# Kernel tuning notes

Hardware: AMD Instinct MI355X
Metric: run time of the kernel (lower is better)

Reference implementation:

```python
import jax, jax.numpy as jnp
import numpy as np

NUM_HEADS = 12
KEEP_RATE = 0.7
EPS = 1e-5  # torch nn.LayerNorm default


def layernorm(x, w, b):
    m = x.mean(-1, keepdims=True)
    v = ((x - m) ** 2).mean(-1, keepdims=True)
    return (x - m) * jax.lax.rsqrt(v + EPS) * w + b


def complement_idx(idx, dim):
    # idx: (B, L) top-k indices into [0, dim). Returns (B, dim-L) sorted complement,
    # matching EViT's scatter-zeros-then-sort trick.
    a = jnp.broadcast_to(jnp.arange(dim, dtype=idx.dtype), idx.shape[:-1] + (dim,))
    masked = jax.vmap(lambda ar, ix: ar.at[ix].set(0))(a, idx)
    n_idx = idx.shape[-1]
    return jnp.sort(masked, axis=-1)[..., n_idx:]


def setup_inputs() -> dict:
    key = jax.random.key(0)
    ks = jax.random.split(key, 8)
    B, N, C = 128, 197, 768
    H = 4 * C
    std = 0.02
    return {
        "x": jax.random.normal(ks[0], (B, N, C), jnp.float32),
        "norm1_w": jnp.ones((C,), jnp.float32),
        "norm1_b": jnp.zeros((C,), jnp.float32),
        "qkv_w": jax.random.normal(ks[1], (C, 3 * C), jnp.float32) * std,  # qkv_bias=False
        "proj_w": jax.random.normal(ks[2], (C, C), jnp.float32) * std,
        "proj_b": jnp.zeros((C,), jnp.float32),
        "norm2_w": jnp.ones((C,), jnp.float32),
        "norm2_b": jnp.zeros((C,), jnp.float32),
        "fc1_w": jax.random.normal(ks[3], (C, H), jnp.float32) * std,
        "fc1_b": jnp.zeros((H,), jnp.float32),
        "fc2_w": jax.random.normal(ks[4], (H, C), jnp.float32) * std,
        "fc2_b": jnp.zeros((C,), jnp.float32),
    }


def reference(x, norm1_w, norm1_b, qkv_w, proj_w, proj_b,
              norm2_w, norm2_b, fc1_w, fc1_b, fc2_w, fc2_b):
    B, N, C = x.shape
    h = NUM_HEADS
    d = C // h
    scale = d ** -0.5

    # ---- Attention (eval mode, no dropout) ----
    xn = layernorm(x, norm1_w, norm1_b)
    qkv = (xn @ qkv_w).reshape(B, N, 3, h, d).transpose(2, 0, 3, 1, 4)
    q, k, v = qkv[0], qkv[1], qkv[2]  # (B, h, N, d)
    attn = jax.nn.softmax(jnp.einsum('bhqd,bhkd->bhqk', q, k) * scale, axis=-1)
    out = jnp.einsum('bhqk,bhkd->bhqd', attn, v).transpose(0, 2, 1, 3).reshape(B, N, C)
    x = x + (out @ proj_w + proj_b)

    # ---- Top-k token selection (keep_rate < 1) ----
    left = int(np.ceil(KEEP_RATE * (N - 1)))          # 138 kept patch tokens
    cls_attn = attn[:, :, 0, 1:].mean(axis=1)         # (B, N-1)
    _, idx = jax.lax.top_k(cls_attn, left)            # sorted descending, like torch.topk
    compl = complement_idx(idx, N - 1)                # (B, M), M = N-1-left

    non_cls = x[:, 1:]                                # (B, N-1, C)
    gather = lambda arr, ix: jnp.take_along_axis(arr, ix[..., None], axis=1)

    x_others = gather(non_cls, idx)                   # (B, L, C)
    non_topk = gather(non_cls, compl)                 # (B, M, C)
    xo_n = x_others / jnp.linalg.norm(x_others, axis=-1, keepdims=True)
    nt_n = non_topk / jnp.linalg.norm(non_topk, axis=-1, keepdims=True)
    distance = jnp.einsum('bmc,blc->bml', nt_n, xo_n)  # cosine similarity (B, M, L)

    # attention-weighted merge of pruned tokens into nearest kept token
    non_cls_w = non_cls * cls_attn[..., None]
    x_others = gather(non_cls_w, idx)
    non_topk = gather(non_cls_w, compl)
    topk_attn = jnp.take_along_axis(cls_attn, idx, axis=1)       # (B, L)
    non_topk_attn = jnp.take_along_axis(cls_attn, compl, axis=1)  # (B, M)
    node_idx = jnp.argmax(distance, axis=-1)                      # (B, M)

    topk_attn = jax.vmap(lambda t, ni, nt: t.at[ni].add(nt))(topk_attn, node_idx, non_topk_attn)
    x_others = jax.vmap(lambda xo, ni, nt: xo.at[ni].add(nt))(x_others, node_idx, non_topk)
    x_others = x_others / topk_attn[..., None]

    x = jnp.concatenate([x[:, :1], x_others], axis=1)  # (B, L+1, C)

    # ---- MLP ----
    xn2 = layernorm(x, norm2_w, norm2_b)
    hmid = jax.nn.gelu(xn2 @ fc1_w + fc1_b, approximate=False)
    x = x + (hmid @ fc2_w + fc2_b)
    return x
```

## Files before the change

### kernel.cpp

```cpp
#include <hip/hip_runtime.h>
#include <math.h>

#define B_ 128
#define N_ 197
#define C_ 768
#define H_ 12
#define D_ 64
#define KEEP_ 138
#define COMP_ 58
#define NOUT_ 139
#define HID_ 3072

typedef __attribute__((ext_vector_type(8))) short bf16x8;
typedef __attribute__((ext_vector_type(8))) _Float16 f16x8;
typedef __attribute__((ext_vector_type(4))) float f32x4;
typedef unsigned short us;

__device__ inline us f2bf(float f) {
    unsigned u = __float_as_uint(f);
    unsigned r = (u + 0x7FFFu + ((u >> 16) & 1u)) >> 16;
    return (us)r;
}
__device__ inline float bf2f(us h) { return __uint_as_float(((unsigned)h) << 16); }
__device__ inline void gload_lds16(const void* g, void* l) {
    __builtin_amdgcn_global_load_lds((const __attribute__((address_space(1))) void*)g,
                                     (__attribute__((address_space(3))) void*)l, 16, 0, 0);
}
__device__ inline void split3(float v, us& h1, us& h2, us& h3) {
    h1 = f2bf(v);
    float r1 = v - bf2f(h1);
    h2 = f2bf(r1);
    h3 = f2bf(r1 - bf2f(h2));
}
__device__ inline void split2h(float v, us& h1, us& h2) {
    float av = fabsf(v);
    float v1 = (av < 6.103515625e-05f) ? 0.f : v;
    _Float16 a = (_Float16)v1;
    float r = (v - (float)a) * 4096.0f;
    _Float16 b = (_Float16)r;
    h1 = *reinterpret_cast<us*>(&a);
    h2 = *reinterpret_cast<us*>(&b);
}

#define WAITV(n) asm volatile("s_waitcnt vmcnt(" #n ")" ::: "memory")
#define RBAR __builtin_amdgcn_s_barrier()

__global__ __launch_bounds__(256) void ln_split2h_kernel(const float* __restrict__ x,
                                                         const float* __restrict__ w,
                                                         const float* __restrict__ bias,
                                                         us* __restrict__ y1,
                                                         us* __restrict__ y2) {
    int row = blockIdx.x;
    const float* xr = x + (size_t)row * C_;
    int tid = threadIdx.x;
    float v[3];
    float s = 0.f, sq = 0.f;
#pragma unroll
    for (int i = 0; i < 3; i++) {
        v[i] = xr[tid + i * 256];
        s += v[i];
        sq += v[i] * v[i];
    }
    __shared__ float s1[256], s2[256];
    s1[tid] = s; s2[tid] = sq;
    __syncthreads();
    for (int o = 128; o > 0; o >>= 1) {
        if (tid < o) { s1[tid] += s1[tid + o]; s2[tid] += s2[tid + o]; }
        __syncthreads();
    }
    float mean = s1[0] * (1.0f / C_);
    float var = s2[0] * (1.0f / C_) - mean * mean;
    float rstd = rsqrtf(var + 1e-5f);
#pragma unroll
    for (int i = 0; i < 3; i++) {
        int c = tid + i * 256;
        float y = (v[i] - mean) * rstd * w[c] + bias[c];
        us h1, h2;
        split2h(y, h1, h2);
        size_t o = (size_t)row * C_ + c;
        y1[o] = h1; y2[o] = h2;
    }
}

__global__ __launch_bounds__(256) void ln2bf_kernel(const float* __restrict__ x,
                                                    const float* __restrict__ w,
                                                    const float* __restrict__ bias,
                                                    us* __restrict__ y) {
    int row = blockIdx.x;
    const float* xr = x + (size_t)row * C_;
    us* yr = y + (size_t)row * C_;
    int tid = threadIdx.x;
    float v[3];
    float s = 0.f, sq = 0.f;
#pragma unroll
    for (int i = 0; i < 3; i++) {
        v[i] = xr[tid + i * 256];
        s += v[i];
        sq += v[i] * v[i];
    }
    __shared__ float s1[256], s2[256];
    s1[tid] = s; s2[tid] = sq;
    __syncthreads();
    for (int o = 128; o > 0; o >>= 1) {
        if (tid < o) { s1[tid] += s1[tid + o]; s2[tid] += s2[tid + o]; }
        __syncthreads();
    }
    float mean = s1[0] * (1.0f / C_);
    float var = s2[0] * (1.0f / C_) - mean * mean;
    float rstd = rsqrtf(var + 1e-5f);
#pragma unroll
    for (int i = 0; i < 3; i++) {
        int c = tid + i * 256;
        yr[c] = f2bf((v[i] - mean) * rstd * w[c] + bias[c]);
    }
}

__global__ __launch_bounds__(256) void wtrans_kernel(const float* __restrict__ in,
                                                     us* __restrict__ out,
                                                     int K, int N) {
    __shared__ float T[32][33];
    int n0 = blockIdx.x * 32, k0 = blockIdx.y * 32;
    int tx = threadIdx.x & 31, ty = threadIdx.x >> 5;
    for (int i = 0; i < 32; i += 8)
        T[ty + i][tx] = in[(size_t)(k0 + ty + i) * N + n0 + tx];
    __syncthreads();
    for (int i = 0; i < 32; i += 8)
        out[(size_t)(n0 + ty + i) * K + k0 + tx] = f2bf(T[tx][ty + i]);
}

__global__ __launch_bounds__(256) void wtrans_split2h_kernel(const float* __restrict__ in,
                                                             us* __restrict__ o1,
                                                             us* __restrict__ o2,
                                                             int K, int N) {
    __shared__ float T[32][33];
    int n0 = blockIdx.x * 32, k0 = blockIdx.y * 32;
    int tx = threadIdx.x & 31, ty = threadIdx.x >> 5;
    for (int i = 0; i < 32; i += 8)
        T[ty + i][tx] = in[(size_t)(k0 + ty + i) * N + n0 + tx];
    __syncthreads();
    for (int i = 0; i < 32; i += 8) {
        us h1, h2;
        split2h(T[tx][ty + i], h1, h2);
        size_t o = (size_t)(n0 + ty + i) * K + k0 + tx;
        o1[o] = h1; o2[o] = h2;
    }
}

template <bool BIAS, bool RES>
__global__ __launch_bounds__(256, 2) void bgemm3h_kernel(const us* __restrict__ A1,
                                                         const us* __restrict__ A2,
                                                         const us* __restrict__ B1,
                                                         const us* __restrict__ B2,
                                                         const float* __restrict__ bias,
                                                         const float* __restrict__ res,
                                                         float* __restrict__ Cm,
                                                         int M, int N, int K) {
    __shared__ short As[2][128 * 64];
    __shared__ short Bs[2][128 * 64];
    int tid = threadIdx.x;
    int lane = tid & 63, wid = tid >> 6;
    int wr = wid >> 1, wc = wid & 1;
    int lr = lane & 15, g = lane >> 4;
    int brow = blockIdx.y * 128, bcol = blockIdx.x * 128;

    f32x4 acc0[4][4] = {};
    f32x4 acc1[4][4] = {};

    for (int k0 = 0; k0 < K; k0 += 64) {
#pragma unroll
        for (int v = 0; v < 4; v++) {
            int rowb = v * 32 + wid * 8;
            int r = rowb + (lane >> 3);
            int slot = lane & 7;
            int chunk = slot ^ (r & 7);
            int garow = brow + r; if (garow >= M) garow = M - 1;
            int gbrow = bcol + r;
            gload_lds16(A1 + (size_t)garow * K + k0 + chunk * 8, &As[0][rowb * 64]);
            gload_lds16(A2 + (size_t)garow * K + k0 + chunk * 8, &As[1][rowb * 64]);
            gload_lds16(B1 + (size_t)gbrow * K + k0 + chunk * 8, &Bs[0][rowb * 64]);
            gload_lds16(B2 + (size_t)gbrow * K + k0 + chunk * 8, &Bs[1][rowb * 64]);
        }
        __syncthreads();
#pragma unroll
        for (int kk = 0; kk < 2; kk++) {
            f16x8 af[2][4], bfr[2][4];
#pragma unroll
            for (int fi = 0; fi < 4; fi++) {
                int ra = wr * 64 + fi * 16 + lr;
                int sla = (kk * 4 + g) ^ (ra & 7);
                int rb = wc * 64 + fi * 16 + lr;
                int slb = (kk * 4 + g) ^ (rb & 7);
#pragma unroll
                for (int s = 0; s < 2; s++) {
                    af[s][fi] = *reinterpret_cast<const f16x8*>(&As[s][ra * 64 + sla * 8]);
                    bfr[s][fi] = *reinterpret_cast<const f16x8*>(&Bs[s][rb * 64 + slb * 8]);
                }
            }
#pragma unroll
            for (int fi = 0; fi < 4; fi++)
#pragma unroll
                for (int fj = 0; fj < 4; fj++) {
                    acc0[fi][fj] = __builtin_amdgcn_mfma_f32_16x16x32_f16(af[0][fi], bfr[0][fj], acc0[fi][fj], 0, 0, 0);
                    acc1[fi][fj] = __builtin_amdgcn_mfma_f32_16x16x32_f16(af[0][fi], bfr[1][fj], acc1[fi][fj], 0, 0, 0);
                    acc1[fi][fj] = __builtin_amdgcn_mfma_f32_16x16x32_f16(af[1][fi], bfr[0][fj], acc1[fi][fj], 0, 0, 0);
                }
        }
        __syncthreads();
    }
#pragma unroll
    for (int fi = 0; fi < 4; fi++) {
#pragma unroll
        for (int fj = 0; fj < 4; fj++) {
            int col = bcol + wc * 64 + fj * 16 + lr;
            float bv = BIAS ? bias[col] : 0.f;
#pragma unroll
            for (int i = 0; i < 4; i++) {
                int r = brow + wr * 64 + fi * 16 + g * 4 + i;
                if (r < M) {
                    float vv = acc0[fi][fj][i] + acc1[fi][fj][i] * (1.0f / 4096.0f) + bv;
                    if (RES) vv += res[(size_t)r * N + col];
                    Cm[(size_t)r * N + col] = vv;
                }
            }
        }
    }
}

template <bool GELU_, bool OUTBF, bool RES>
__global__ __launch_bounds__(256, 3) void bgemm_kernel(const us* __restrict__ A,
                                                       const us* __restrict__ Bt,
                                                       const float* __restrict__ bias,
                                                       const float* __restrict__ res,
                                                       void* __restrict__ Cout,
                                                       int M, int N, int K) {
    __shared__ short As0[128 * 32];
    __shared__ short Bs0[128 * 32];
    __shared__ short As1[128 * 32];
    __shared__ short Bs1[128 * 32];
    int tid = threadIdx.x;
    int lane = tid & 63, wid = tid >> 6;
    int wr = wid >> 1, wc = wid & 1;
    int lr = lane & 15, g = lane >> 4;
    int brow = blockIdx.y * 128, bcol = blockIdx.x * 128;
    int lrow = lane >> 2, lslot = lane & 3;
    const int sa = (g ^ (lr & 3)) * 8;

    f32x4 acc[4][4] = {};

    auto stage = [&](short (&Aa)[128 * 32], short (&Bb)[128 * 32], int k0) {
#pragma unroll
        for (int v = 0; v < 2; v++) {
            int rowb = wid * 32 + v * 16;
            int ra = rowb + lrow;
            int hsel = (lslot ^ (ra & 3)) * 8;
            int garow = brow + ra; if (garow >= M) garow = M - 1;
            gload_lds16(A + (size_t)garow * K + k0 + hsel, &Aa[rowb * 32]);
            gload_lds16(Bt + (size_t)(bcol + ra) * K + k0 + hsel, &Bb[rowb * 32]);
        }
    };
    auto compute = [&](short (&Aa)[128 * 32], short (&Bb)[128 * 32]) {
        bf16x8 af[4], bfr[4];
#pragma unroll
        for (int fi = 0; fi < 4; fi++)
            af[fi] = *reinterpret_cast<const bf16x8*>(&Aa[(wr * 64 + fi * 16 + lr) * 32 + sa]);
#pragma unroll
        for (int fj = 0; fj < 4; fj++)
            bfr[fj] = *reinterpret_cast<const bf16x8*>(&Bb[(wc * 64 + fj * 16 + lr) * 32 + sa]);
#pragma unroll
        for (int fi = 0; fi < 4; fi++)
#pragma unroll
            for (int fj = 0; fj < 4; fj++)
                acc[fi][fj] = __builtin_amdgcn_mfma_f32_16x16x32_bf16(af[fi], bfr[fj], acc[fi][fj], 0, 0, 0);
    };

    stage(As0, Bs0, 0);
    for (int k0 = 0; k0 < K; k0 += 64) {
        if (k0 + 32 < K) {
            stage(As1, Bs1, k0 + 32);
            WAITV(4);
        } else {
            WAITV(0);
        }
        RBAR;
        compute(As0, Bs0);
        RBAR;
        if (k0 + 64 < K) {
            stage(As0, Bs0, k0 + 64);
            WAITV(4);
        } else {
            WAITV(0);
        }
        RBAR;
        compute(As1, Bs1);
        RBAR;
    }
#pragma unroll
    for (int fi = 0; fi < 4; fi++) {
#pragma unroll
        for (int fj = 0; fj < 4; fj++) {
            int col = bcol + wc * 64 + fj * 16 + lr;
            float bv = bias[col];
#pragma unroll
            for (int i = 0; i < 4; i++) {
                int r = brow + wr * 64 + fi * 16 + g * 4 + i;
                if (r < M) {
                    float vv = acc[fi][fj][i] + bv;
                    if (GELU_) vv = 0.5f * vv * (1.0f + erff(vv * 0.70710678118654752f));
                    if (OUTBF) {
                        ((us*)Cout)[(size_t)r * N + col] = f2bf(vv);
                    } else {
                        if (RES) vv += res[(size_t)r * N + col];
                        ((float*)Cout)[(size_t)r * N + col] = vv;
                    }
                }
            }
        }
    }
}

__global__ __launch_bounds__(512, 1) void attn11_kernel(const float* __restrict__ qkv,
                                                        us* __restrict__ ao1,
                                                        us* __restrict__ ao2,
                                                        float* __restrict__ attn0,
                                                        int b0) {
    int hh = blockIdx.x, b = blockIdx.y;
    int tid = threadIdx.x, lane = tid & 63, wv = tid >> 6;
    int lr = lane & 15, g = lane >> 4;
    __shared__ short Ks[3][208 * 64];
    __shared__ short Vt[2][64 * 224];
    __shared__ unsigned Pscr[8][16 * 32];
    const size_t base = (size_t)b * N_ * 3 * C_ + (size_t)hh * D_;

    for (int i = tid; i < 208 * 8; i += 512) {
        int k = i >> 3, oct = i & 7;
        int d0 = (oct ^ (k & 7)) * 8;
        float tv[8];
        if (k < N_) {
            const float4* kp = reinterpret_cast<const float4*>(qkv + base + (size_t)k * 3 * C_ + C_ + d0);
            float4 aa = kp[0], bb = kp[1];
            tv[0] = aa.x; tv[1] = aa.y; tv[2] = aa.z; tv[3] = aa.w;
            tv[4] = bb.x; tv[5] = bb.y; tv[6] = bb.z; tv[7] = bb.w;
        } else {
#pragma unroll
            for (int e = 0; e < 8; e++) tv[e] = 0.f;
        }
        bf16x8 h1v, h2v, h3v;
#pragma unroll
        for (int e = 0; e < 8; e++) {
            us ha, hb, hc;
            split3(tv[e], ha, hb, hc);
            h1v[e] = (short)ha; h2v[e] = (short)hb; h3v[e] = (short)hc;
        }
        int di = k * 64 + oct * 8;
        *reinterpret_cast<bf16x8*>(&Ks[0][di]) = h1v;
        *reinterpret_cast<bf16x8*>(&Ks[1][di]) = h2v;
        *reinterpret_cast<bf16x8*>(&Ks[2][di]) = h3v;
    }
    {
        int d = tid & 63, jb = tid >> 6;
        for (int it = 0; it < 28; it++) {
            int k = it * 8 + jb;
            float vv = (k < N_) ? qkv[base + (size_t)k * 3 * C_ + 2 * C_ + d] : 0.f;
            us p1 = f2bf(vv);
            us p2 = f2bf(vv - bf2f(p1));
            int idx = d * 224 + (((k >> 3) ^ (d & 3)) * 8) + (k & 7);
            Vt[0][idx] = (short)p1;
            Vt[1][idx] = (short)p2;
        }
    }
    __syncthreads();

#pragma unroll
    for (int chunk = 0; chunk < 2; chunk++) {
        int qbase = chunk * 128 + wv * 16;
        bf16x8 qf1[2], qf2[2], qf3[2];
        int qrow = qbase + lr;
#pragma unroll
        for (int kk = 0; kk < 2; kk++) {
            float qv[8];
            if (qrow < N_) {
                const float4* qp = reinterpret_cast<const float4*>(qkv + base + (size_t)qrow * 3 * C_ + kk * 32 + g * 8);
                float4 aa = qp[0], bb = qp[1];
                qv[0] = aa.x; qv[1] = aa.y; qv[2] = aa.z; qv[3] = aa.w;
                qv[4] = bb.x; qv[5] = bb.y; qv[6] = bb.z; qv[7] = bb.w;
            } else {
#pragma unroll
                for (int e = 0; e < 8; e++) qv[e] = 0.f;
            }
#pragma unroll
            for (int e = 0; e < 8; e++) {
                us ha, hb, hc;
                split3(qv[e], ha, hb, hc);
                qf1[kk][e] = (short)ha; qf2[kk][e] = (short)hb; qf3[kk][e] = (short)hc;
            }
        }
        f32x4 sacc[13] = {};
#pragma unroll
        for (int kt = 0; kt < 13; kt++) {
#pragma unroll
            for (int kk = 0; kk < 2; kk++) {
                int row = kt * 16 + lr;
                int sl = ((kk * 4 + g) ^ (row & 7)) * 8;
                const bf16x8 b1 = *reinterpret_cast<const bf16x8*>(&Ks[0][row * 64 + sl]);
                const bf16x8 b2 = *reinterpret_cast<const bf16x8*>(&Ks[1][row * 64 + sl]);
                const bf16x8 b3 = *reinterpret_cast<const bf16x8*>(&Ks[2][row * 64 + sl]);
                sacc[kt] = __builtin_amdgcn_mfma_f32_16x16x32_bf16(qf1[kk], b1, sacc[kt], 0, 0, 0);
                sacc[kt] = __builtin_amdgcn_mfma_f32_16x16x32_bf16(qf1[kk], b2, sacc[kt], 0, 0, 0);
                sacc[kt] = __builtin_amdgcn_mfma_f32_16x16x32_bf16(qf2[kk], b1, sacc[kt], 0, 0, 0);
                sacc[kt] = __builtin_amdgcn_mfma_f32_16x16x32_bf16(qf1[kk], b3, sacc[kt], 0, 0, 0);
                sacc[kt] = __builtin_amdgcn_mfma_f32_16x16x32_bf16(qf3[kk], b1, sacc[kt], 0, 0, 0);
                sacc[kt] = __builtin_amdgcn_mfma_f32_16x16x32_bf16(qf2[kk], b2, sacc[kt], 0, 0, 0);
            }
        }
#pragma unroll
        for (int i = 0; i < 4; i++) {
            float m = -1e30f;
#pragma unroll
            for (int kt = 0; kt < 13; kt++) {
                int k = kt * 16 + lr;
                float lgv = (k < N_) ? sacc[kt][i] * 0.125f : -1e30f;
                sacc[kt][i] = lgv;
                m = fmaxf(m, lgv);
            }
            m = fmaxf(m, __shfl_xor(m, 1, 64));
            m = fmaxf(m, __shfl_xor(m, 2, 64));
            m = fmaxf(m, __shfl_xor(m, 4, 64));
            m = fmaxf(m, __shfl_xor(m, 8, 64));
            float se = 0.f;
#pragma unroll
            for (int kt = 0; kt < 13; kt++) {
                int k = kt * 16 + lr;
                float e = (k < N_) ? expf(sacc[kt][i] - m) : 0.f;
                sacc[kt][i] = e;
                se += e;
            }
            se += __shfl_xor(se, 1, 64);
            se += __shfl_xor(se, 2, 64);
            se += __shfl_xor(se, 4, 64);
            se += __shfl_xor(se, 8, 64);
            float inv = 1.0f / se;
#pragma unroll
            for (int kt = 0; kt < 13; kt++) sacc[kt][i] *= inv;
        }
        if (chunk == 0 && wv == 0 && g == 0) {
#pragma unroll
            for (int kt = 0; kt < 13; kt++) {
                int k = kt * 16 + lr;
                if (k < N_) attn0[((size_t)(b0 + b) * H_ + hh) * N_ + k] = sacc[kt][0];
            }
        }
        f32x4 oacc[4] = {};
#pragma unroll
        for (int sect = 0; sect < 7; sect++) {
#pragma unroll
            for (int t = 0; t < 2; t++) {
                int kt = sect * 2 + t;
#pragma unroll
                for (int i = 0; i < 4; i++) {
                    float p = (kt < 13) ? sacc[kt][i] : 0.f;
                    us h1 = f2bf(p);
                    us h2 = f2bf(p - bf2f(h1));
                    Pscr[wv][(g * 4 + i) * 32 + t * 16 + lr] = (unsigned)h1 | ((unsigned)h2 << 16);
                }
            }
            uint4 u0 = *reinterpret_cast<const uint4*>(&Pscr[wv][lr * 32 + g * 8]);
            uint4 u1 = *reinterpret_cast<const uint4*>(&Pscr[wv][lr * 32 + g * 8 + 4]);
            unsigned uu[8] = {u0.x, u0.y, u0.z, u0.w, u1.x, u1.y, u1.z, u1.w};
            bf16x8 pa1, pa2;
#pragma unroll
            for (int e = 0; e < 8; e++) {
                pa1[e] = (short)(uu[e] & 0xffffu);
                pa2[e] = (short)(uu[e] >> 16);
            }
#pragma unroll
            for (int dt = 0; dt < 4; dt++) {
                int row = dt * 16 + lr;
                int cc = sect * 4 + g;
                int idx = row * 224 + ((cc ^ (row & 3)) * 8);
                const bf16x8 v1 = *reinterpret_cast<const bf16x8*>(&Vt[0][idx]);
                const bf16x8 v2 = *reinterpret_cast<const bf16x8*>(&Vt[1][idx]);
                oacc[dt] = __builtin_amdgcn_mfma_f32_16x16x32_bf16(pa1, v1, oacc[dt], 0, 0, 0);
                oacc[dt] = __builtin_amdgcn_mfma_f32_16x16x32_bf16(pa1, v2, oacc[dt], 0, 0, 0);
                oacc[dt] = __builtin_amdgcn_mfma_f32_16x16x32_bf16(pa2, v1, oacc[dt], 0, 0, 0);
            }
        }
#pragma unroll
        for (int dt = 0; dt < 4; dt++) {
#pragma unroll
            for (int i = 0; i < 4; i++) {
                int q = qbase + g * 4 + i;
                if (q < N_) {
                    int d = dt * 16 + lr;
                    size_t oi = ((size_t)(b * N_ + q)) * C_ + (size_t)hh * D_ + d;
                    us h1, h2;
                    split2h(oacc[dt][i], h1, h2);
                    ao1[oi] = h1; ao2[oi] = h2;
                }
            }
        }
    }
}

__global__ __launch_bounds__(256) void cls_kernel(const float* __restrict__ attn0,
                                                  float* __restrict__ cls) {
    int b = blockIdx.x, tid = threadIdx.x;
    if (tid < N_ - 1) {
        float s = 0.f;
        for (int hh = 0; hh < H_; hh++) s += attn0[((size_t)b * H_ + hh) * N_ + 1 + tid];
        cls[b * (N_ - 1) + tid] = s * (1.0f / H_);
    }
}

__global__ __launch_bounds__(256) void topk_kernel(const float* __restrict__ cls,
                                                   int* __restrict__ idx,
                                                   int* __restrict__ cmp) {
    int b = blockIdx.x, tid = threadIdx.x;
    __shared__ float vals[196];
    __shared__ int rk[196];
    if (tid < 196) vals[tid] = cls[b * 196 + tid];
    __syncthreads();
    if (tid < 196) {
        float v = vals[tid];
        int r = 0;
        for (int j = 0; j < 196; j++) {
            float u = vals[j];
            r += (u > v) || (u == v && j < tid);
        }
        rk[tid] = r;
    }
    __syncthreads();
    if (tid < 196) {
        int r = rk[tid];
        if (r < KEEP_) {
            idx[b * KEEP_ + r] = tid;
        } else {
            int pos = 0;
            for (int j = 0; j < tid; j++) pos += (rk[j] >= KEEP_);
            cmp[b * COMP_ + pos] = tid;
        }
    }
}

__global__ __launch_bounds__(256) void rnorm_kernel(const float* __restrict__ x1,
                                                    float* __restrict__ rn) {
    int i = blockIdx.x, b = blockIdx.y, tid = threadIdx.x;
    const float* xr = x1 + ((size_t)b * N_ + 1 + i) * C_;
    float sq = 0.f;
#pragma unroll
    for (int k = 0; k < 3; k++) {
        float v = xr[tid + k * 256];
        sq += v * v;
    }
    __shared__ float s2[256];
    s2[tid] = sq;
    __syncthreads();
    for (int o = 128; o > 0; o >>= 1) {
        if (tid < o) s2[tid] += s2[tid + o];
        __syncthreads();
    }
    if (tid == 0) rn[b * 196 + i] = rsqrtf(s2[0]);
}

__global__ __launch_bounds__(256) void dist2_kernel(const float* __restrict__ x1,
                                                    const float* __restrict__ rn,
                                                    const int* __restrict__ idx,
                                                    const int* __restrict__ cmp,
                                                    int* __restrict__ node) {
    int b = blockIdx.x, tid = threadIdx.x;
    __shared__ float As2[64][65];
    __shared__ float Bs2[64][145];
    __shared__ float Ds[COMP_][KEEP_ + 1];
    __shared__ int cpl[COMP_];
    __shared__ int til[KEEP_];
    __shared__ float rnt[KEEP_];
    if (tid < COMP_) cpl[tid] = cmp[b * COMP_ + tid];
    if (tid < KEEP_) {
        int t = idx[b * KEEP_ + tid];
        til[tid] = t;
        rnt[tid] = rn[b * 196 + t];
    }
    __syncthreads();
    int tr = tid >> 4, tc = tid & 15;
    float acc[4][9] = {};
    for (int k0 = 0; k0 < C_; k0 += 64) {
        for (int ii = tid; ii < COMP_ * 64; ii += 256) {
            int l = ii >> 6, k = ii & 63;
            As2[k][l] = x1[((size_t)b * N_ + 1 + cpl[l]) * C_ + k0 + k];
        }
        for (int ii = tid; ii < KEEP_ * 64; ii += 256) {
            int m = ii >> 6, k = ii & 63;
            Bs2[k][m] = x1[((size_t)b * N_ + 1 + til[m]) * C_ + k0 + k];
        }
        __syncthreads();
#pragma unroll 4
        for (int k = 0; k < 64; k++) {
            float ar[4], br[9];
#pragma unroll
            for (int i = 0; i < 4; i++) ar[i] = As2[k][tr * 4 + i];
#pragma unroll
            for (int j = 0; j < 9; j++) br[j] = Bs2[k][tc * 9 + j];
#pragma unroll
            for (int i = 0; i < 4; i++)
#pragma unroll
                for (int j = 0; j < 9; j++) acc[i][j] += ar[i] * br[j];
        }
        __syncthreads();
    }
#pragma unroll
    for (int i = 0; i < 4; i++) {
        int l = tr * 4 + i;
        if (l < COMP_) {
#pragma unroll
            for (int j = 0; j < 9; j++) {
                int m = tc * 9 + j;
                if (m < KEEP_) Ds[l][m] = acc[i][j] * rnt[m];
            }
        }
    }
    __syncthreads();
    if (tid < COMP_) {
        float best = -1e30f; int bm = 0;
        for (int m = 0; m < KEEP_; m++) {
            float dv = Ds[tid][m];
            if (dv > best) { best = dv; bm = m; }
        }
        node[b * COMP_ + tid] = bm;
    }
}

__global__ __launch_bounds__(256) void fuse_kernel(const float* __restrict__ x1,
                                                   const float* __restrict__ cls,
                                                   const int* __restrict__ idx,
                                                   const int* __restrict__ cmp,
                                                   const int* __restrict__ node,
                                                   float* __restrict__ x2) {
    int mr = blockIdx.x, b = blockIdx.y, tid = threadIdx.x;
    if (mr == 0) {
        for (int c = tid; c < C_; c += 256)
            x2[(size_t)b * NOUT_ * C_ + c] = x1[(size_t)b * N_ * C_ + c];
        return;
    }
    int m = mr - 1;
    __shared__ int nds[COMP_];
    __shared__ int cps[COMP_];
    if (tid < COMP_) {
        nds[tid] = node[b * COMP_ + tid];
        cps[tid] = cmp[b * COMP_ + tid];
    }
    __syncthreads();
    int ti = idx[b * KEEP_ + m];
    float ta = cls[b * 196 + ti];
    float denom = ta;
    for (int l = 0; l < COMP_; l++)
        if (nds[l] == m) denom += cls[b * 196 + cps[l]];
    float a[3];
    const float* xr = x1 + ((size_t)b * N_ + 1 + ti) * C_;
#pragma unroll
    for (int i = 0; i < 3; i++) a[i] = xr[tid + i * 256] * ta;
    for (int l = 0; l < COMP_; l++) {
        if (nds[l] == m) {
            float ca = cls[b * 196 + cps[l]];
            const float* yr = x1 + ((size_t)b * N_ + 1 + cps[l]) * C_;
#pragma unroll
            for (int i = 0; i < 3; i++) a[i] += yr[tid + i * 256] * ca;
        }
    }
    float invd = 1.0f / denom;
#pragma unroll
    for (int i = 0; i < 3; i++)
        x2[((size_t)b * NOUT_ + mr) * C_ + tid + i * 256] = a[i] * invd;
}

extern "C" void kernel_launch(void* const* d_in, const int* in_sizes, int n_in,
                              void* d_out, int out_size, void* d_ws, size_t ws_size,
                              hipStream_t stream) {
    const float* x       = (const float*)d_in[0];
    const float* norm1_w = (const float*)d_in[1];
    const float* norm1_b = (const float*)d_in[2];
    const float* qkv_w   = (const float*)d_in[3];
    const float* proj_w  = (const float*)d_in[4];
    const float* proj_b  = (const float*)d_in[5];
    const float* norm2_w = (const float*)d_in[6];
    const float* norm2_b = (const float*)d_in[7];
    const float* fc1_w   = (const float*)d_in[8];
    const float* fc1_b   = (const float*)d_in[9];
    const float* fc2_w   = (const float*)d_in[10];
    const float* fc2_b   = (const float*)d_in[11];
    float* out = (float*)d_out;

    const int M1 = B_ * N_;
    const int M2 = B_ * NOUT_;
    const size_t WT_F  = 2359296;
    const size_t C3C   = (size_t)C_ * 3 * C_;
    const size_t CC    = (size_t)C_ * C_;

    const size_t small_f = (size_t)B_ * H_ * N_ + 2u * B_ * 196;
    const size_t small_i = (size_t)B_ * KEEP_ + 2u * B_ * COMP_;
    const size_t x1_f = (size_t)M1 * C_;

    const int cb_t[4] = {64, 32, 16, 4};
    const int rm_t[4] = {M2, M2, 4864, 320};
    int CB = 4, RMLP = 320;
    size_t scr_f = 0;
    {
        bool ok = false;
        for (int tier = 0; tier < 4; tier++) {
            int cb = cb_t[tier], rm = rm_t[tier];
            size_t cbnc = (size_t)cb * N_ * C_;
            size_t front_f = (C3C + CC) + cbnc + 3 * cbnc;
            size_t mlp_f   = WT_F + (size_t)rm * 1920;
            size_t sf      = front_f > mlp_f ? front_f : mlp_f;
            size_t nd      = (x1_f + sf + small_f) * 4 + small_i * 4;
            if (ws_size >= nd) { CB = cb; RMLP = rm; scr_f = sf; ok = true; break; }
        }
        if (!ok) return;
    }

    float* ws = (float*)d_ws;
    float* x1    = ws;
    float* scr   = x1 + x1_f;
    float* attn0 = scr + scr_f;
    float* cls   = attn0 + (size_t)B_ * H_ * N_;
    float* rn    = cls + B_ * 196;
    int* idxb    = (int*)(rn + B_ * 196);
    int* cmpb    = idxb + B_ * KEEP_;
    int* nodeb   = cmpb + B_ * COMP_;
    float* x2    = out;

    const size_t cbnc = (size_t)CB * N_ * C_;
    us* sb  = (us*)scr;
    us* qw1 = sb;            us* qw2 = qw1 + C3C;
    us* pw1 = qw2 + C3C;     us* pw2 = pw1 + CC;
    us* xn1 = pw2 + CC;      us* xn2 = xn1 + cbnc;
    float* qkv_c = (float*)(xn2 + cbnc);
    us* ao1 = xn1;  us* ao2 = xn2;
    us* fc1wt  = (us*)scr;
    us* fc2wt  = fc1wt + (size_t)C_ * HID_;
    us* xn2bf  = fc2wt + (size_t)C_ * HID_;
    us* hmidbf = xn2bf + (size_t)RMLP * C_;

    wtrans_split2h_kernel<<<dim3(3 * C_ / 32, C_ / 32), 256, 0, stream>>>(qkv_w, qw1, qw2, C_, 3 * C_);
    wtrans_split2h_kernel<<<dim3(C_ / 32, C_ / 32), 256, 0, stream>>>(proj_w, pw1, pw2, C_, C_);

    for (int b0 = 0; b0 < B_; b0 += CB) {
        int cb = (B_ - b0 < CB) ? (B_ - b0) : CB;
        int Mc = cb * N_;
        const float* xch = x + (size_t)b0 * N_ * C_;
        ln_split2h_kernel<<<Mc, 256, 0, stream>>>(xch, norm1_w, norm1_b, xn1, xn2);
        bgemm3h_kernel<false, false><<<dim3(3 * C_ / 128, (Mc + 127) / 128), 256, 0, stream>>>(
            xn1, xn2, qw1, qw2, nullptr, nullptr, qkv_c, Mc, 3 * C_, C_);
        attn11_kernel<<<dim3(H_, cb), 512, 0, stream>>>(qkv_c, ao1, ao2, attn0, b0);
        bgemm3h_kernel<true, true><<<dim3(C_ / 128, (Mc + 127) / 128), 256, 0, stream>>>(
            ao1, ao2, pw1, pw2, proj_b, xch, x1 + (size_t)b0 * N_ * C_, Mc, C_, C_);
    }

    cls_kernel<<<B_, 256, 0, stream>>>(attn0, cls);
    topk_kernel<<<B_, 256, 0, stream>>>(cls, idxb, cmpb);
    rnorm_kernel<<<dim3(196, B_), 256, 0, stream>>>(x1, rn);
    dist2_kernel<<<B_, 256, 0, stream>>>(x1, rn, idxb, cmpb, nodeb);
    fuse_kernel<<<dim3(NOUT_, B_), 256, 0, stream>>>(x1, cls, idxb, cmpb, nodeb, x2);

    wtrans_kernel<<<dim3(HID_ / 32, C_ / 32), 256, 0, stream>>>(fc1_w, fc1wt, C_, HID_);
    wtrans_kernel<<<dim3(C_ / 32, HID_ / 32), 256, 0, stream>>>(fc2_w, fc2wt, HID_, C_);

    for (int r0 = 0; r0 < M2; r0 += RMLP) {
        int R = M2 - r0 < RMLP ? M2 - r0 : RMLP;
        ln2bf_kernel<<<R, 256, 0, stream>>>(x2 + (size_t)r0 * C_, norm2_w, norm2_b, xn2bf);
        bgemm_kernel<true, true, false><<<dim3(HID_ / 128, (R + 127) / 128), 256, 0, stream>>>(
            xn2bf, fc1wt, fc1_b, nullptr, hmidbf, R, HID_, C_);
        bgemm_kernel<false, false, true><<<dim3(C_ / 128, (R + 127) / 128), 256, 0, stream>>>(
            hmidbf, fc2wt, fc2_b, x2 + (size_t)r0 * C_, out + (size_t)r0 * C_, R, C_, HID_);
    }
}
```

Before: 1.485 ms.

## Split cosine-distance kernel across two blocks per batch with warp-shuffle argmax

The distance/argmax kernel now launches two blocks per batch, each handling 29 of the 58 pruned tokens, which doubles the grid from 128 to 256 blocks. Each thread computes a 4x5 tile instead of 4x9, reads the A fragment with a float4 LDS load, and finds the argmax by wavefront shuffle reduction instead of writing a shared distance matrix and scanning it serially. The cost is that both blocks reload the same kept-token rows, so global traffic for those rows doubles. The kernel is a small part of the total runtime.

```diff
diff --git a/kernel.cpp b/kernel.cpp
--- a/kernel.cpp
+++ b/kernel.cpp
@@ -561,29 +561,30 @@
     if (tid == 0) rn[b * 196 + i] = rsqrtf(s2[0]);
 }
 
-__global__ __launch_bounds__(256) void dist2_kernel(const float* __restrict__ x1,
-                                                    const float* __restrict__ rn,
-                                                    const int* __restrict__ idx,
-                                                    const int* __restrict__ cmp,
-                                                    int* __restrict__ node) {
-    int b = blockIdx.x, tid = threadIdx.x;
-    __shared__ float As2[64][65];
-    __shared__ float Bs2[64][145];
-    __shared__ float Ds[COMP_][KEEP_ + 1];
-    __shared__ int cpl[COMP_];
+__global__ __launch_bounds__(256, 3) void dist3_kernel(const float* __restrict__ x1,
+                                                       const float* __restrict__ rn,
+                                                       const int* __restrict__ idx,
+                                                       const int* __restrict__ cmp,
+                                                       int* __restrict__ node) {
+    int b = blockIdx.x, half = blockIdx.y;
+    int l0 = half * 29;
+    int tid = threadIdx.x;
+    __shared__ __align__(16) float As2[64][36];
+    __shared__ float Bs2[64][161];
+    __shared__ int cpl[29];
     __shared__ int til[KEEP_];
     __shared__ float rnt[KEEP_];
-    if (tid < COMP_) cpl[tid] = cmp[b * COMP_ + tid];
+    if (tid < 29) cpl[tid] = cmp[b * COMP_ + l0 + tid];
     if (tid < KEEP_) {
         int t = idx[b * KEEP_ + tid];
         til[tid] = t;
         rnt[tid] = rn[b * 196 + t];
     }
     __syncthreads();
-    int tr = tid >> 4, tc = tid & 15;
-    float acc[4][9] = {};
+    int tr = tid >> 5, tc = tid & 31;
+    float acc[4][5] = {};
     for (int k0 = 0; k0 < C_; k0 += 64) {
-        for (int ii = tid; ii < COMP_ * 64; ii += 256) {
+        for (int ii = tid; ii < 29 * 64; ii += 256) {
             int l = ii >> 6, k = ii & 63;
             As2[k][l] = x1[((size_t)b * N_ + 1 + cpl[l]) * C_ + k0 + k];
         }
@@ -594,37 +595,38 @@
         __syncthreads();
 #pragma unroll 4
         for (int k = 0; k < 64; k++) {
-            float ar[4], br[9];
-#pragma unroll
-            for (int i = 0; i < 4; i++) ar[i] = As2[k][tr * 4 + i];
-#pragma unroll
-            for (int j = 0; j < 9; j++) br[j] = Bs2[k][tc * 9 + j];
+            float ar[4], br[5];
+            *reinterpret_cast<float4*>(ar) = *reinterpret_cast<const float4*>(&As2[k][tr * 4]);
+#pragma unroll
+            for (int j = 0; j < 5; j++) br[j] = Bs2[k][tc * 5 + j];
 #pragma unroll
             for (int i = 0; i < 4; i++)
 #pragma unroll
-                for (int j = 0; j < 9; j++) acc[i][j] += ar[i] * br[j];
+                for (int j = 0; j < 5; j++) acc[i][j] += ar[i] * br[j];
         }
         __syncthreads();
     }
 #pragma unroll
     for (int i = 0; i < 4; i++) {
-        int l = tr * 4 + i;
-        if (l < COMP_) {
-#pragma unroll
-            for (int j = 0; j < 9; j++) {
-                int m = tc * 9 + j;
-                if (m < KEEP_) Ds[l][m] = acc[i][j] * rnt[m];
-            }
-        }
-    }
-    __syncthreads();
-    if (tid < COMP_) {
-        float best = -1e30f; int bm = 0;
-        for (int m = 0; m < KEEP_; m++) {
-            float dv = Ds[tid][m];
-            if (dv > best) { best = dv; bm = m; }
-        }
-        node[b * COMP_ + tid] = bm;
+        int ll = tr * 4 + i;
+        if (ll < 29) {
+            float best = -3.0e38f;
+            int bm = 0x7fffffff;
+#pragma unroll
+            for (int j = 0; j < 5; j++) {
+                int m = tc * 5 + j;
+                if (m < KEEP_) {
+                    float dv = acc[i][j] * rnt[m];
+                    if (dv > best) { best = dv; bm = m; }
+                }
+            }
+            for (int o = 1; o < 32; o <<= 1) {
+                float ov = __shfl_xor(best, o, 64);
+                int oi = __shfl_xor(bm, o, 64);
+                if (ov > best || (ov == best && oi < bm)) { best = ov; bm = oi; }
+            }
+            if (tc == 0) node[b * COMP_ + l0 + ll] = bm;
+        }
     }
 }
 
@@ -757,7 +759,7 @@
     cls_kernel<<<B_, 256, 0, stream>>>(attn0, cls);
     topk_kernel<<<B_, 256, 0, stream>>>(cls, idxb, cmpb);
     rnorm_kernel<<<dim3(196, B_), 256, 0, stream>>>(x1, rn);
-    dist2_kernel<<<B_, 256, 0, stream>>>(x1, rn, idxb, cmpb, nodeb);
+    dist3_kernel<<<dim3(B_, 2), 256, 0, stream>>>(x1, rn, idxb, cmpb, nodeb);
     fuse_kernel<<<dim3(NOUT_, B_), 256, 0, stream>>>(x1, cls, idxb, cmpb, nodeb, x2);
 
     wtrans_kernel<<<dim3(HID_ / 32, C_ / 32), 256, 0, stream>>>(fc1_w, fc1wt, C_, HID_);
```

New measurement: 1.429 ms. 3.8% less time.
